# Performance work log

Measured on AMD Instinct MI355X. Metric: run time of the kernel, lower is better.

The kernel has to match this reference:

```python
import jax, jax.numpy as jnp
import numpy as np

N_EMBD = 768
N_HEADS = 12

def setup_inputs() -> dict:
    key = jax.random.key(0)
    ks = jax.random.split(key, 5)
    B, T, C = 8, 1024, N_EMBD
    s_in = 1.0 / np.sqrt(C)
    x = jax.random.normal(ks[0], (B, T, C), dtype=jnp.float32)
    W_attn = jax.random.normal(ks[1], (C, 3 * C), dtype=jnp.float32) * s_in
    b_attn = jnp.zeros((3 * C,), dtype=jnp.float32)
    W_proj = jax.random.normal(ks[2], (C, C), dtype=jnp.float32) * s_in
    b_proj = jnp.zeros((C,), dtype=jnp.float32)
    return {"x": x, "W_attn": W_attn, "b_attn": b_attn, "W_proj": W_proj, "b_proj": b_proj}

def reference(x, W_attn, b_attn, W_proj, b_proj):
    B, T, C = x.shape
    H = N_HEADS
    hd = C // H
    qkv = x @ W_attn + b_attn                      # [B,T,3C]
    q, k, v = jnp.split(qkv, 3, axis=-1)
    # [B,T,C] -> [B,H,T,hd]
    q = q.reshape(B, T, H, hd).transpose(0, 2, 1, 3)
    k = k.reshape(B, T, H, hd).transpose(0, 2, 1, 3)
    v = v.reshape(B, T, H, hd).transpose(0, 2, 1, 3)
    att = jnp.einsum('bhqd,bhkd->bhqk', q, k) * (1.0 / np.sqrt(hd))
    mask = jnp.tril(jnp.ones((T, T), dtype=bool))
    att = jnp.where(mask, att, -jnp.inf)
    att = jax.nn.softmax(att, axis=-1)
    y = jnp.einsum('bhqk,bhkd->bhqd', att, v)      # [B,H,T,hd]
    y = y.transpose(0, 2, 1, 3).reshape(B, T, C)
    return y @ W_proj + b_proj
```

## Files before the change

### kernel.cpp

```cpp
#include <hip/hip_runtime.h>
#include <hip/hip_bf16.h>
#include <cmath>

typedef __bf16 bf16_t;
typedef __bf16 bf16x8 __attribute__((ext_vector_type(8)));
typedef float f32x4 __attribute__((ext_vector_type(4)));

#define MFMA16(A, B, C) __builtin_amdgcn_mfma_f32_16x16x32_bf16(A, B, C, 0, 0, 0)

#define GLOAD_LDS16(g, l)                                                      \
  __builtin_amdgcn_global_load_lds(                                            \
      (const __attribute__((address_space(1))) void*)(g),                      \
      (__attribute__((address_space(3))) void*)(l), 16, 0, 0)

__global__ __launch_bounds__(256) void prep(
    const float* __restrict__ x, bf16_t* __restrict__ xb,
    const float* __restrict__ Wa, bf16_t* __restrict__ wta,
    const float* __restrict__ Wp, bf16_t* __restrict__ wtp) {
  __shared__ bf16_t tile[32][33];
  const int id = blockIdx.x;
  if (id < 3072) {
    const size_t i = (size_t)id * 256 + threadIdx.x;
    const float4 a0 = ((const float4*)x)[i * 2];
    const float4 a1 = ((const float4*)x)[i * 2 + 1];
    bf16x8 v = {(bf16_t)a0.x, (bf16_t)a0.y, (bf16_t)a0.z, (bf16_t)a0.w,
                (bf16_t)a1.x, (bf16_t)a1.y, (bf16_t)a1.z, (bf16_t)a1.w};
    ((bf16x8*)xb)[i] = v;
    return;
  }
  const float* src;
  bf16_t* dst;
  int R, C, c0, r0;
  if (id < 3072 + 1728) {
    const int t = id - 3072;
    src = Wa; dst = wta; R = 768; C = 2304;
    c0 = (t % 72) * 32; r0 = (t / 72) * 32;
  } else {
    const int t = id - 4800;
    src = Wp; dst = wtp; R = 768; C = 768;
    c0 = (t % 24) * 32; r0 = (t / 24) * 32;
  }
  const int tr = threadIdx.x >> 5;
  const int tc = threadIdx.x & 31;
#pragma unroll
  for (int i = 0; i < 32; i += 8)
    tile[tr + i][tc] = (bf16_t)src[(size_t)(r0 + tr + i) * C + (c0 + tc)];
  __syncthreads();
#pragma unroll
  for (int i = 0; i < 32; i += 8)
    dst[(size_t)(c0 + tr + i) * R + (r0 + tc)] = tile[tc][tr + i];
}

__global__ __launch_bounds__(768, 1) void gemm_qkv(
    const bf16_t* __restrict__ A, const bf16_t* __restrict__ BT,
    const float* __restrict__ bias,
    bf16_t* __restrict__ o0, bf16_t* __restrict__ o1, bf16_t* __restrict__ o2,
    int K) {
  extern __shared__ __align__(16) bf16_t smem[];
  constexpr int ASZ = 256 * 64;
  constexpr int BSZ = 288 * 64;
  bf16_t* Bbase = smem + 2 * ASZ;

  const int tid = threadIdx.x;
  const int w = tid >> 6, lane = tid & 63;
  const int wr = w / 6, wc = w % 6;
  const int quad = lane >> 4, l16 = lane & 15;

  const int id = blockIdx.x;
  const int xcd = id & 7;
  const int lin = id >> 3;
  const int nt = lin & 7;
  const int mt = (xcd << 2) + (lin >> 3);

  const int dr = lane >> 3;
  const int dc = (((lane & 7) - dr) & 7) << 3;

  const int so0 = ((quad + (l16 & 7)) & 7) << 3;
  const int so1 = so0 ^ 32;

  f32x4 acc[8][3] = {};

  auto stage = [&](int t, int s) {
    const size_t ko = (size_t)t * 64 + dc;
#pragma unroll
    for (int j = 0; j < 6; ++j) {
      const int u = w + j * 12;
      if (u < 32) {
        GLOAD_LDS16(A + (size_t)(mt * 256 + u * 8 + dr) * K + ko,
                    smem + s * ASZ + u * 8 * 64);
      } else if (u < 68) {
        const int v = u - 32;
        GLOAD_LDS16(BT + (size_t)(nt * 288 + v * 8 + dr) * K + ko,
                    Bbase + s * BSZ + v * 8 * 64);
      }
    }
  };

  auto compute = [&](int s) {
#pragma unroll
    for (int ks = 0; ks < 2; ++ks) {
      const int so = ks ? so1 : so0;
      bf16x8 bfrag[3], afrag[8];
#pragma unroll
      for (int ni = 0; ni < 3; ++ni)
        bfrag[ni] = *(const bf16x8*)(Bbase + s * BSZ +
                                     (wc * 48 + ni * 16 + l16) * 64 + so);
#pragma unroll
      for (int mi = 0; mi < 8; ++mi)
        afrag[mi] = *(const bf16x8*)(smem + s * ASZ +
                                     (wr * 128 + mi * 16 + l16) * 64 + so);
      __builtin_amdgcn_s_setprio(1);
#pragma unroll
      for (int mi = 0; mi < 8; ++mi)
#pragma unroll
        for (int ni = 0; ni < 3; ++ni)
          acc[mi][ni] = MFMA16(afrag[mi], bfrag[ni], acc[mi][ni]);
      __builtin_amdgcn_s_setprio(0);
    }
  };

  const int NIT = K / 64;
  stage(0, 0);
  __syncthreads();
  for (int t = 0; t < NIT; ++t) {
    if (t + 1 < NIT) stage(t + 1, (t + 1) & 1);
    compute(t & 1);
    if (t + 1 < NIT) __syncthreads();
  }

  const int m_base = mt * 256 + wr * 128;
  const int n_base = nt * 288 + wc * 48;
#pragma unroll
  for (int ni = 0; ni < 3; ++ni) {
    const int n = n_base + ni * 16 + l16;
    const float bv = bias[n];
    const int which = n / 768;
    const int c = n - which * 768;
    const int h = c >> 6, d = c & 63;
#pragma unroll
    for (int mi = 0; mi < 8; ++mi) {
#pragma unroll
      for (int r = 0; r < 4; ++r) {
        const int m = m_base + mi * 16 + quad * 4 + r;
        const bf16_t bw = (bf16_t)(acc[mi][ni][r] + bv);
        const int b = m >> 10, t = m & 1023;
        const size_t bh = (size_t)(b * 12 + h);
        if (which == 0)
          o0[(bh * 1024 + t) * 64 + d] = bw;
        else if (which == 1)
          o1[(bh * 1024 + t) * 64 + d] = bw;
        else
          o2[(bh * 64 + d) * 1024 + t] = bw;
      }
    }
  }
}

__global__ __launch_bounds__(256) void gemm_proj(
    const bf16_t* __restrict__ A, const bf16_t* __restrict__ BT,
    const float* __restrict__ bias, float* __restrict__ of, int N, int K) {
  constexpr int BM = 128, BN = 128, BK = 32;
  __shared__ __align__(16) bf16_t As[2][BM][BK];
  __shared__ __align__(16) bf16_t Bs[2][BN][BK];

  const int tid = threadIdx.x;
  const int wave = tid >> 6, lane = tid & 63;
  const int wr = wave >> 1, wc = wave & 1;
  const int quad = lane >> 4, l16 = lane & 15;

  const int id = blockIdx.x;
  const int xcd = id & 7;
  const int lin = id >> 3;
  const int nt = lin % 6;
  const int mt = xcd * 8 + lin / 6;

  const int rl = lane >> 2;
  const int cq = ((lane & 3) - (rl >> 1)) & 3;
  const int ac = cq << 3;
  const bf16_t* Ag0 = A + (size_t)(mt * BM + wave * 32 + rl) * K + ac;
  const bf16_t* Ag1 = Ag0 + (size_t)16 * K;
  const bf16_t* Bg0 = BT + (size_t)(nt * BN + wave * 32 + rl) * K + ac;
  const bf16_t* Bg1 = Bg0 + (size_t)16 * K;

  const int sw = ((quad + (l16 >> 1)) & 3) << 3;

  f32x4 acc[4][4] = {};

  auto stage = [&](int k0, int buf) {
    GLOAD_LDS16(Ag0 + k0, &As[buf][wave * 32][0]);
    GLOAD_LDS16(Ag1 + k0, &As[buf][wave * 32 + 16][0]);
    GLOAD_LDS16(Bg0 + k0, &Bs[buf][wave * 32][0]);
    GLOAD_LDS16(Bg1 + k0, &Bs[buf][wave * 32 + 16][0]);
  };
  auto compute = [&](int buf) {
    bf16x8 af[4], bfr[4];
#pragma unroll
    for (int mi = 0; mi < 4; ++mi)
      af[mi] = *(const bf16x8*)(&As[buf][wr * 64 + mi * 16 + l16][sw]);
#pragma unroll
    for (int ni = 0; ni < 4; ++ni)
      bfr[ni] = *(const bf16x8*)(&Bs[buf][wc * 64 + ni * 16 + l16][sw]);
#pragma unroll
    for (int mi = 0; mi < 4; ++mi)
#pragma unroll
      for (int ni = 0; ni < 4; ++ni)
        acc[mi][ni] = MFMA16(af[mi], bfr[ni], acc[mi][ni]);
  };

  const int NIT = K / BK;
  stage(0, 0);
  for (int k = 0; k + 2 < NIT; k += 2) {
    __syncthreads();
    stage((k + 1) * BK, 1);
    compute(0);
    __syncthreads();
    stage((k + 2) * BK, 0);
    compute(1);
  }
  __syncthreads();
  stage((NIT - 1) * BK, 1);
  compute(0);
  __syncthreads();
  compute(1);

  const int m_base = mt * BM + wr * 64;
  const int n_base = nt * BN + wc * 64;
#pragma unroll
  for (int ni = 0; ni < 4; ++ni) {
    const int n = n_base + ni * 16 + l16;
    const float bv = bias[n];
#pragma unroll
    for (int mi = 0; mi < 4; ++mi)
#pragma unroll
      for (int r = 0; r < 4; ++r) {
        const int m = m_base + mi * 16 + quad * 4 + r;
        of[(size_t)m * N + n] = acc[mi][ni][r] + bv;
      }
  }
}

__global__ __launch_bounds__(256, 3) void attn_fwd(
    const bf16_t* __restrict__ Q, const bf16_t* __restrict__ Kg,
    const bf16_t* __restrict__ VT, bf16_t* __restrict__ Y) {
  __shared__ __align__(16) bf16_t Ks[2][64][64];
  __shared__ __align__(16) bf16_t Vs[2][64][64];
  __shared__ __align__(16) bf16_t Ps[4][16][72];

  const int tid = threadIdx.x;
  const int w = tid >> 6, lane = tid & 63;
  const int quad = lane >> 4, l16 = lane & 15;

  const int id = blockIdx.x;
  const int xcd = id & 7;
  const int lin = id >> 3;
  const int pair = lin & 7;
  const int h = lin >> 3;
  const int b = xcd;
  const size_t bh = (size_t)(b * 12 + h);
  const bf16_t* Qbh = Q + bh * 65536;
  const bf16_t* Kbh = Kg + bh * 65536;
  const bf16_t* VTbh = VT + bh * 65536;

  const int drow = lane >> 3;
  const int dchunk = (((lane & 7) - drow) & 7) << 3;

  const int so0 = ((quad + (l16 & 7)) & 7) << 3;
  const int so1 = so0 ^ 32;

  constexpr float SC = 0.18033688011112042f;
  constexpr float FM = 12.0f;
  const bf16_t one_b = (bf16_t)1.0f;
  const bf16x8 ones = {one_b, one_b, one_b, one_b,
                       one_b, one_b, one_b, one_b};

  auto stageKV = [&](int kt, int bufi) {
#pragma unroll
    for (int j = 0; j < 2; ++j) {
      const int r = w * 16 + j * 8 + drow;
      GLOAD_LDS16(Kbh + (size_t)(kt * 64 + r) * 64 + dchunk,
                  &Ks[bufi][w * 16 + j * 8][0]);
      GLOAD_LDS16(VTbh + (size_t)r * 1024 + kt * 64 + dchunk,
                  &Vs[bufi][w * 16 + j * 8][0]);
    }
  };

  const int qtb = 15 - pair;
  const int qts = pair;

  const int qrb = qtb * 64 + w * 16 + l16;
  const int qrs = qts * 64 + w * 16 + l16;
  const bf16x8 qb0 = *(const bf16x8*)(Qbh + (size_t)qrb * 64 + quad * 8);
  const bf16x8 qb1 = *(const bf16x8*)(Qbh + (size_t)qrb * 64 + 32 + quad * 8);
  const bf16x8 qs0 = *(const bf16x8*)(Qbh + (size_t)qrs * 64 + quad * 8);
  const bf16x8 qs1 = *(const bf16x8*)(Qbh + (size_t)qrs * 64 + 32 + quad * 8);

  f32x4 ob[5] = {};
  f32x4 os[5] = {};

  auto compute_q = [&](f32x4* o, const bf16x8& q0, const bf16x8& q1,
                       int bufi, bool diag) {
    f32x4 s[4];
#pragma unroll
    for (int ni = 0; ni < 4; ++ni) {
      bf16x8 kf0 = *(const bf16x8*)(&Ks[bufi][ni * 16 + l16][so0]);
      bf16x8 kf1 = *(const bf16x8*)(&Ks[bufi][ni * 16 + l16][so1]);
      f32x4 t = {};
      t = MFMA16(q0, kf0, t);
      t = MFMA16(q1, kf1, t);
      s[ni] = t;
    }
    if (diag) {
#pragma unroll
      for (int ni = 0; ni < 4; ++ni)
#pragma unroll
        for (int r = 0; r < 4; ++r) {
          const int kp = ni * 16 + l16;
          const int qr = w * 16 + quad * 4 + r;
          const float p = (kp > qr) ? 0.0f : exp2f(fmaf(s[ni][r], SC, -FM));
          Ps[w][quad * 4 + r][ni * 16 + l16] = (bf16_t)p;
        }
    } else {
#pragma unroll
      for (int ni = 0; ni < 4; ++ni)
#pragma unroll
        for (int r = 0; r < 4; ++r)
          Ps[w][quad * 4 + r][ni * 16 + l16] =
              (bf16_t)exp2f(fmaf(s[ni][r], SC, -FM));
    }
    bf16x8 pf0 = *(const bf16x8*)(&Ps[w][l16][quad * 8]);
    bf16x8 pf1 = *(const bf16x8*)(&Ps[w][l16][32 + quad * 8]);
#pragma unroll
    for (int nd = 0; nd < 4; ++nd) {
      bf16x8 vf0 = *(const bf16x8*)(&Vs[bufi][nd * 16 + l16][so0]);
      bf16x8 vf1 = *(const bf16x8*)(&Vs[bufi][nd * 16 + l16][so1]);
      o[nd] = MFMA16(pf0, vf0, o[nd]);
      o[nd] = MFMA16(pf1, vf1, o[nd]);
    }
    o[4] = MFMA16(pf0, ones, o[4]);
    o[4] = MFMA16(pf1, ones, o[4]);
  };

  stageKV(0, 0);
  int buf = 0;
  for (int kt = 0; kt <= qtb; ++kt) {
    __syncthreads();
    if (kt < qtb) stageKV(kt + 1, buf ^ 1);
    compute_q(ob, qb0, qb1, buf, kt == qtb);
    if (kt <= qts) compute_q(os, qs0, qs1, buf, kt == qts);
    buf ^= 1;
  }

#pragma unroll
  for (int r = 0; r < 4; ++r) {
    const float invb = 1.0f / ob[4][r];
    const int tb = qtb * 64 + w * 16 + quad * 4 + r;
    bf16_t* yb = Y + ((size_t)b * 1024 + tb) * 768 + h * 64;
#pragma unroll
    for (int nd = 0; nd < 4; ++nd)
      yb[nd * 16 + l16] = (bf16_t)(ob[nd][r] * invb);
    const float invs = 1.0f / os[4][r];
    const int ts = qts * 64 + w * 16 + quad * 4 + r;
    bf16_t* ys = Y + ((size_t)b * 1024 + ts) * 768 + h * 64;
#pragma unroll
    for (int nd = 0; nd < 4; ++nd)
      ys[nd * 16 + l16] = (bf16_t)(os[nd][r] * invs);
  }
}

extern "C" void kernel_launch(void* const* d_in, const int* in_sizes, int n_in,
                              void* d_out, int out_size, void* d_ws,
                              size_t ws_size, hipStream_t stream) {
  const float* x      = (const float*)d_in[0];
  const float* W_attn = (const float*)d_in[1];
  const float* b_attn = (const float*)d_in[2];
  const float* W_proj = (const float*)d_in[3];
  const float* b_proj = (const float*)d_in[4];
  float* out = (float*)d_out;

  const size_t HEADS = 96;
  bf16_t* wta = (bf16_t*)d_ws;
  bf16_t* wtp = wta + (size_t)2304 * 768;
  bf16_t* qw  = wtp + (size_t)768 * 768;
  bf16_t* kw  = qw + HEADS * 1024 * 64;
  bf16_t* vtw = kw + HEADS * 1024 * 64;
  bf16_t* yw  = vtw + HEADS * 1024 * 64;
  bf16_t* xb  = yw + (size_t)8192 * 768;

  prep<<<dim3(5376), 256, 0, stream>>>(x, xb, W_attn, wta, W_proj, wtp);
  const size_t qkv_lds = (size_t)(2 * (256 + 288) * 64) * sizeof(bf16_t);
  gemm_qkv<<<dim3(256), 768, qkv_lds, stream>>>(
      xb, wta, b_attn, qw, kw, vtw, 768);
  attn_fwd<<<dim3(768), 256, 0, stream>>>(qw, kw, vtw, yw);
  gemm_proj<<<dim3(384), 256, 0, stream>>>(
      yw, wtp, b_proj, out, 768, 768);
}
```

Baseline: 194.0 us.

## Retile projection GEMM to 128x192 blocks with 12 waves and BK=64

```diff
diff --git a/kernel.cpp b/kernel.cpp
--- a/kernel.cpp
+++ b/kernel.cpp
@@ -156,77 +156,85 @@
   }
 }
 
-__global__ __launch_bounds__(256) void gemm_proj(
+__global__ __launch_bounds__(768, 1) void gemm_proj(
     const bf16_t* __restrict__ A, const bf16_t* __restrict__ BT,
     const float* __restrict__ bias, float* __restrict__ of, int N, int K) {
-  constexpr int BM = 128, BN = 128, BK = 32;
-  __shared__ __align__(16) bf16_t As[2][BM][BK];
-  __shared__ __align__(16) bf16_t Bs[2][BN][BK];
+  extern __shared__ __align__(16) bf16_t smem[];
+  constexpr int ASZ = 128 * 64;
+  constexpr int BSZ = 192 * 64;
+  bf16_t* Bbase = smem + 2 * ASZ;
 
   const int tid = threadIdx.x;
-  const int wave = tid >> 6, lane = tid & 63;
-  const int wr = wave >> 1, wc = wave & 1;
+  const int w = tid >> 6, lane = tid & 63;
+  const int wr = w / 6, wc = w % 6;
   const int quad = lane >> 4, l16 = lane & 15;
 
   const int id = blockIdx.x;
   const int xcd = id & 7;
   const int lin = id >> 3;
-  const int nt = lin % 6;
-  const int mt = xcd * 8 + lin / 6;
-
-  const int rl = lane >> 2;
-  const int cq = ((lane & 3) - (rl >> 1)) & 3;
-  const int ac = cq << 3;
-  const bf16_t* Ag0 = A + (size_t)(mt * BM + wave * 32 + rl) * K + ac;
-  const bf16_t* Ag1 = Ag0 + (size_t)16 * K;
-  const bf16_t* Bg0 = BT + (size_t)(nt * BN + wave * 32 + rl) * K + ac;
-  const bf16_t* Bg1 = Bg0 + (size_t)16 * K;
-
-  const int sw = ((quad + (l16 >> 1)) & 3) << 3;
-
-  f32x4 acc[4][4] = {};
-
-  auto stage = [&](int k0, int buf) {
-    GLOAD_LDS16(Ag0 + k0, &As[buf][wave * 32][0]);
-    GLOAD_LDS16(Ag1 + k0, &As[buf][wave * 32 + 16][0]);
-    GLOAD_LDS16(Bg0 + k0, &Bs[buf][wave * 32][0]);
-    GLOAD_LDS16(Bg1 + k0, &Bs[buf][wave * 32 + 16][0]);
-  };
-  auto compute = [&](int buf) {
-    bf16x8 af[4], bfr[4];
-#pragma unroll
-    for (int mi = 0; mi < 4; ++mi)
-      af[mi] = *(const bf16x8*)(&As[buf][wr * 64 + mi * 16 + l16][sw]);
-#pragma unroll
-    for (int ni = 0; ni < 4; ++ni)
-      bfr[ni] = *(const bf16x8*)(&Bs[buf][wc * 64 + ni * 16 + l16][sw]);
-#pragma unroll
-    for (int mi = 0; mi < 4; ++mi)
-#pragma unroll
-      for (int ni = 0; ni < 4; ++ni)
-        acc[mi][ni] = MFMA16(af[mi], bfr[ni], acc[mi][ni]);
-  };
-
-  const int NIT = K / BK;
+  const int nt = lin & 3;
+  const int mt = (xcd << 3) + (lin >> 2);
+
+  const int dr = lane >> 3;
+  const int dc = (((lane & 7) - dr) & 7) << 3;
+
+  const int so0 = ((quad + (l16 & 7)) & 7) << 3;
+  const int so1 = so0 ^ 32;
+
+  f32x4 acc[4][2] = {};
+
+  auto stage = [&](int t, int s) {
+    const size_t ko = (size_t)t * 64 + dc;
+#pragma unroll
+    for (int j = 0; j < 4; ++j) {
+      const int u = w + j * 12;
+      if (u < 16) {
+        GLOAD_LDS16(A + (size_t)(mt * 128 + u * 8 + dr) * K + ko,
+                    smem + s * ASZ + u * 8 * 64);
+      } else if (u < 40) {
+        const int v = u - 16;
+        GLOAD_LDS16(BT + (size_t)(nt * 192 + v * 8 + dr) * K + ko,
+                    Bbase + s * BSZ + v * 8 * 64);
+      }
+    }
+  };
+
+  auto compute = [&](int s) {
+#pragma unroll
+    for (int ks = 0; ks < 2; ++ks) {
+      const int so = ks ? so1 : so0;
+      bf16x8 bfrag[2], afrag[4];
+#pragma unroll
+      for (int ni = 0; ni < 2; ++ni)
+        bfrag[ni] = *(const bf16x8*)(Bbase + s * BSZ +
+                                     (wc * 32 + ni * 16 + l16) * 64 + so);
+#pragma unroll
+      for (int mi = 0; mi < 4; ++mi)
+        afrag[mi] = *(const bf16x8*)(smem + s * ASZ +
+                                     (wr * 64 + mi * 16 + l16) * 64 + so);
+      __builtin_amdgcn_s_setprio(1);
+#pragma unroll
+      for (int mi = 0; mi < 4; ++mi)
+#pragma unroll
+        for (int ni = 0; ni < 2; ++ni)
+          acc[mi][ni] = MFMA16(afrag[mi], bfrag[ni], acc[mi][ni]);
+      __builtin_amdgcn_s_setprio(0);
+    }
+  };
+
+  const int NIT = K / 64;
   stage(0, 0);
-  for (int k = 0; k + 2 < NIT; k += 2) {
-    __syncthreads();
-    stage((k + 1) * BK, 1);
-    compute(0);
-    __syncthreads();
-    stage((k + 2) * BK, 0);
-    compute(1);
-  }
   __syncthreads();
-  stage((NIT - 1) * BK, 1);
-  compute(0);
-  __syncthreads();
-  compute(1);
-
-  const int m_base = mt * BM + wr * 64;
-  const int n_base = nt * BN + wc * 64;
-#pragma unroll
-  for (int ni = 0; ni < 4; ++ni) {
+  for (int t = 0; t < NIT; ++t) {
+    if (t + 1 < NIT) stage(t + 1, (t + 1) & 1);
+    compute(t & 1);
+    if (t + 1 < NIT) __syncthreads();
+  }
+
+  const int m_base = mt * 128 + wr * 64;
+  const int n_base = nt * 192 + wc * 32;
+#pragma unroll
+  for (int ni = 0; ni < 2; ++ni) {
     const int n = n_base + ni * 16 + l16;
     const float bv = bias[n];
 #pragma unroll
@@ -391,6 +399,7 @@
   gemm_qkv<<<dim3(256), 768, qkv_lds, stream>>>(
       xb, wta, b_attn, qw, kw, vtw, 768);
   attn_fwd<<<dim3(768), 256, 0, stream>>>(qw, kw, vtw, yw);
-  gemm_proj<<<dim3(384), 256, 0, stream>>>(
+  const size_t proj_lds = (size_t)(2 * (128 + 192) * 64) * sizeof(bf16_t);
+  gemm_proj<<<dim3(256), 768, proj_lds, stream>>>(
       yw, wtp, b_proj, out, 768, 768);
 }
```

After: 190.4 us. Within noise of the previous version (-1.9%).
